# Kernel tuning notes

Measured on AMD Instinct MI355X. Metric: run time of the kernel, lower is better.

## Reference

```python
import jax, jax.numpy as jnp
import numpy as np

NUM_NODES = 100000
NUM_EDGES = 6400000


def setup_inputs() -> dict:
    key = jax.random.key(0)
    k1, k2 = jax.random.split(key)
    e = jax.random.normal(k1, (NUM_EDGES,), dtype=jnp.float32)
    edge_index = jax.random.randint(k2, (2, NUM_EDGES), 0, NUM_NODES, dtype=jnp.int64 if jax.config.jax_enable_x64 else jnp.int32)
    return {"e": e, "edge_index": edge_index, "num_nodes": NUM_NODES}


def reference(e, edge_index, num_nodes):
    # GAT edge softmax (no max-subtraction, matching the 'simple' variant)
    target_nodes = edge_index[1]                      # [E]
    exp_e = jnp.exp(e)                                # [E]
    sum_exp = jax.ops.segment_sum(exp_e, target_nodes, num_segments=num_nodes)  # [N]
    alpha = exp_e / (sum_exp[target_nodes] + 1e-16)   # gather + normalize
    return alpha
```

## Files before the change

kernel.cpp:

```cpp
#include <hip/hip_runtime.h>


typedef unsigned long long ull;

#define NB 25
#define CHUNK_LG 12
#define CHUNK (1 << CHUNK_LG)
#define CCAP (NB * CHUNK)
#define BBLK 512
#define BIN_THREADS 512
#define NSH 2
#define CAP_SH 384
#define BCAP (NSH * CAP_SH)
#define SB 64
#define SRCPG (BBLK / SB)
#define SCB (NB * SB)
#define SCAT_THREADS 256
#define NSUB 8

#define SUMS_OFF 0u
#define FLAG_OFF (448u * 1024u)
#define SUBS_OFF (512u * 1024u)
#define CNTS_OFF (4u << 20)
#define BUF_OFF  (5u << 20)
#define PART_OFF (45u << 20)

__device__ __forceinline__ unsigned short f32_to_f16_bits(float x) {
    union { _Float16 h; unsigned short u; } cv;
    cv.h = (_Float16)x;
    return cv.u;
}
__device__ __forceinline__ float f16_bits_to_f32(unsigned short u) {
    union { unsigned short u; _Float16 h; } cv;
    cv.u = u;
    return (float)cv.h;
}
__device__ __forceinline__ unsigned pack_edge(int t, float x) {
    return ((unsigned)(t & (CHUNK - 1)) << 16) | (unsigned)f32_to_f16_bits(x);
}

__global__ void zero_flag(unsigned* __restrict__ flag) {
    if (threadIdx.x == 0) *flag = 0u;
}

__global__ __launch_bounds__(BIN_THREADS)
void gat_bin(const float* __restrict__ e, const int* __restrict__ tgt,
             unsigned* __restrict__ buf, unsigned* __restrict__ cnts_t,
             unsigned* __restrict__ flag, int per, int E) {
    __shared__ unsigned stage[NB * NSH * CAP_SH];
    __shared__ unsigned lcnt[NB * NSH];
    __shared__ unsigned lovf;
    const int blk = blockIdx.x;
    const int tid = threadIdx.x;
    if (tid < NB * NSH) lcnt[tid] = 0;
    if (tid == 0) lovf = 0;
    __syncthreads();

    const int sh = tid & (NSH - 1);

    const long long start = (long long)blk * per;
    long long rem = (long long)E - start;
    if (rem < 0) rem = 0;
    int nv = per >> 2;
    if ((long long)nv > (rem >> 2)) nv = (int)(rem >> 2);
    const int tail_lo = nv * 4;
    int tail_hi = per;
    if ((long long)tail_hi > rem) tail_hi = (int)rem;

    const float4* e4 = reinterpret_cast<const float4*>(e + start);
    const int4*  t4 = reinterpret_cast<const int4*>(tgt + start);

#define BIN_ONE(T, X)                                                        \
    {   const int t_ = (T);                                                  \
        const unsigned b_ = (unsigned)t_ >> CHUNK_LG;                        \
        if (b_ < NB) {                                                       \
            const unsigned pk_ = pack_edge(t_, __expf(X));                   \
            const unsigned s_ = atomicAdd(&lcnt[b_ * NSH + sh], 1u);         \
            if (s_ < CAP_SH) stage[(b_ * NSH + sh) * CAP_SH + s_] = pk_;     \
            else lovf = 1;                                                   \
        } else lovf = 1;                                                     \
    }
    for (int v = tid; v < nv; v += BIN_THREADS) {
        const float4 ev = e4[v];
        const int4 tv = t4[v];
        BIN_ONE(tv.x, ev.x)
        BIN_ONE(tv.y, ev.y)
        BIN_ONE(tv.z, ev.z)
        BIN_ONE(tv.w, ev.w)
    }
    for (int i = tail_lo + tid; i < tail_hi; i += BIN_THREADS) {
        BIN_ONE(tgt[start + i], e[start + i])
    }
#undef BIN_ONE
    __syncthreads();

#pragma unroll 5
    for (int b = 0; b < NB; ++b) {
        const unsigned c0 = min(lcnt[b * NSH + 0], (unsigned)CAP_SH);
        const unsigned c1 = min(lcnt[b * NSH + 1], (unsigned)CAP_SH);
        unsigned* dst = buf + ((size_t)blk * NB + b) * BCAP;
        const unsigned* s0 = stage + (size_t)(b * NSH + 0) * CAP_SH;
        const unsigned* s1 = stage + (size_t)(b * NSH + 1) * CAP_SH;
        for (unsigned j = tid; j < c0; j += BIN_THREADS) dst[j] = s0[j];
        for (unsigned j = tid; j < c1; j += BIN_THREADS) dst[c0 + j] = s1[j];
        if (tid == 0) cnts_t[b * BBLK + blk] = c0 + c1;
    }
    if (tid == 0 && lovf) atomicOr(flag, 1u);
}

__global__ __launch_bounds__(SCAT_THREADS)
void gat_scatter_bins(const unsigned* __restrict__ buf,
                      const unsigned* __restrict__ cnts_t,
                      unsigned* __restrict__ partials) {
    __shared__ float hist[CHUNK];
    const int blk = blockIdx.x;
    const int b = blk / SB;
    const int g = blk - b * SB;
    const int tid = threadIdx.x;

    const uint4 ca = *(const uint4*)(cnts_t + b * BBLK + g * SRCPG);
    const uint4 cb = *(const uint4*)(cnts_t + b * BBLK + g * SRCPG + 4);
    int ms[SRCPG] = {(int)ca.x, (int)ca.y, (int)ca.z, (int)ca.w,
                     (int)cb.x, (int)cb.y, (int)cb.z, (int)cb.w};

    float4 z; z.x = z.y = z.z = z.w = 0.0f;
#pragma unroll
    for (int j = tid; j < CHUNK / 4; j += SCAT_THREADS)
        ((float4*)hist)[j] = z;
    __syncthreads();

#pragma unroll
    for (int s = 0; s < SRCPG; ++s) {
        const int sb = g * SRCPG + s;
        const int m = ms[s];
        const unsigned* src = buf + ((size_t)sb * NB + b) * BCAP;
        const int nv = m >> 2;
        const uint4* s4 = (const uint4*)src;
        for (int v = tid; v < nv; v += SCAT_THREADS) {
            const uint4 q = s4[v];
            atomicAdd(&hist[q.x >> 16], f16_bits_to_f32((unsigned short)q.x));
            atomicAdd(&hist[q.y >> 16], f16_bits_to_f32((unsigned short)q.y));
            atomicAdd(&hist[q.z >> 16], f16_bits_to_f32((unsigned short)q.z));
            atomicAdd(&hist[q.w >> 16], f16_bits_to_f32((unsigned short)q.w));
        }
        for (int i = nv * 4 + tid; i < m; i += SCAT_THREADS) {
            const unsigned q = src[i];
            atomicAdd(&hist[q >> 16], f16_bits_to_f32((unsigned short)q));
        }
    }
    __syncthreads();

    uint4* dst = (uint4*)(partials + (size_t)blk * (CHUNK / 2));
    const float4* h4 = (const float4*)hist;
#pragma unroll
    for (int j = tid; j < CHUNK / 8; j += SCAT_THREADS) {
        const float4 a = h4[2 * j];
        const float4 c = h4[2 * j + 1];
        uint4 o;
        o.x = (unsigned)f32_to_f16_bits(a.x) | ((unsigned)f32_to_f16_bits(a.y) << 16);
        o.y = (unsigned)f32_to_f16_bits(a.z) | ((unsigned)f32_to_f16_bits(a.w) << 16);
        o.z = (unsigned)f32_to_f16_bits(c.x) | ((unsigned)f32_to_f16_bits(c.y) << 16);
        o.w = (unsigned)f32_to_f16_bits(c.z) | ((unsigned)f32_to_f16_bits(c.w) << 16);
        dst[j] = o;
    }
}

__global__ void gat_reduce1(const unsigned short* __restrict__ partials,
                            float* __restrict__ subsums) {
    const int per_sub = CCAP >> 2;
    const int t = blockIdx.x * blockDim.x + threadIdx.x;
    if (t >= per_sub * NSUB) return;
    const int sub = t / per_sub;
    const int r = t - sub * per_sub;
    const int nd = r << 2;
    const int b = nd >> CHUNK_LG;
    const int w = nd & (CHUNK - 1);
    const int blk0 = b * SB + sub * (SB / NSUB);
    const unsigned short* p = partials + ((size_t)blk0 * CHUNK) + w;
    float a0 = 0.f, a1 = 0.f, a2 = 0.f, a3 = 0.f;
#pragma unroll
    for (int s = 0; s < SB / NSUB; ++s) {
        const ushort4 v = *(const ushort4*)(p + (size_t)s * CHUNK);
        a0 += f16_bits_to_f32(v.x); a1 += f16_bits_to_f32(v.y);
        a2 += f16_bits_to_f32(v.z); a3 += f16_bits_to_f32(v.w);
    }
    float4 o; o.x = a0; o.y = a1; o.z = a2; o.w = a3;
    *(float4*)(subsums + (size_t)sub * CCAP + nd) = o;
}

__global__ void gat_reduce2(const float* __restrict__ subsums,
                            const int* __restrict__ np,
                            float* __restrict__ sums) {
    const int n = *np;
    const int q = blockIdx.x * blockDim.x + threadIdx.x;
    const int nd = q * 4;
    if (nd >= CCAP) return;
    float4 acc; acc.x = acc.y = acc.z = acc.w = 0.f;
#pragma unroll
    for (int s = 0; s < NSUB; ++s) {
        const float4 v = *(const float4*)(subsums + (size_t)s * CCAP + nd);
        acc.x += v.x; acc.y += v.y; acc.z += v.z; acc.w += v.w;
    }
    if (nd + 4 <= n) {
        *(float4*)(sums + nd) = acc;
    } else {
        if (nd     < n) sums[nd]     = acc.x;
        if (nd + 1 < n) sums[nd + 1] = acc.y;
        if (nd + 2 < n) sums[nd + 2] = acc.z;
        if (nd + 3 < n) sums[nd + 3] = acc.w;
    }
}

__global__ void fb_zero(float* __restrict__ sums,
                        const unsigned* __restrict__ flag) {
    if (*flag == 0u) return;
    const int stride = gridDim.x * blockDim.x;
    for (int i = blockIdx.x * blockDim.x + threadIdx.x; i < CCAP; i += stride)
        sums[i] = 0.0f;
}

__global__ void fb_scatter(const float4* __restrict__ e4,
                           const int4* __restrict__ t4,
                           const float* __restrict__ e,
                           const int* __restrict__ tgt,
                           float* __restrict__ sums,
                           const unsigned* __restrict__ flag,
                           int n4, int E) {
    if (*flag == 0u) return;
    const int stride = gridDim.x * blockDim.x;
    const int tid = blockIdx.x * blockDim.x + threadIdx.x;
    for (int i = tid; i < n4; i += stride) {
        const float4 ev = e4[i];
        const int4 tv = t4[i];
        if ((unsigned)tv.x < (unsigned)CCAP) atomicAdd(&sums[tv.x], __expf(ev.x));
        if ((unsigned)tv.y < (unsigned)CCAP) atomicAdd(&sums[tv.y], __expf(ev.y));
        if ((unsigned)tv.z < (unsigned)CCAP) atomicAdd(&sums[tv.z], __expf(ev.z));
        if ((unsigned)tv.w < (unsigned)CCAP) atomicAdd(&sums[tv.w], __expf(ev.w));
    }
    const int tail_base = n4 * 4;
    for (int i = tail_base + tid; i < E; i += stride) {
        const int t = tgt[i];
        if ((unsigned)t < (unsigned)CCAP) atomicAdd(&sums[t], __expf(e[i]));
    }
}

__global__ void gat_zero_sums(float* __restrict__ sums,
                              const int* __restrict__ np) {
    const int n = *np;
    const int stride = gridDim.x * blockDim.x;
    for (int i = blockIdx.x * blockDim.x + threadIdx.x; i < n; i += stride)
        sums[i] = 0.0f;
}

__global__ void gat_exp_scatter(const float4* __restrict__ e4,
                                const int4* __restrict__ t4,
                                const float* __restrict__ e,
                                const int* __restrict__ tgt,
                                float* __restrict__ sums,
                                int n4, int E) {
    const int stride = gridDim.x * blockDim.x;
    const int tid = blockIdx.x * blockDim.x + threadIdx.x;
    for (int i = tid; i < n4; i += stride) {
        const float4 ev = e4[i];
        const int4 tv = t4[i];
        atomicAdd(&sums[tv.x], __expf(ev.x));
        atomicAdd(&sums[tv.y], __expf(ev.y));
        atomicAdd(&sums[tv.z], __expf(ev.z));
        atomicAdd(&sums[tv.w], __expf(ev.w));
    }
    const int tail_base = n4 * 4;
    if (tid < E - tail_base)
        atomicAdd(&sums[tgt[tail_base + tid]], __expf(e[tail_base + tid]));
}

__global__ void gat_normalize(const float4* __restrict__ e4,
                              const int4* __restrict__ t4,
                              const float* __restrict__ e,
                              const int* __restrict__ tgt,
                              const float* __restrict__ sums,
                              float4* __restrict__ out4,
                              float* __restrict__ out,
                              int n4, int E) {
    const int stride = gridDim.x * blockDim.x;
    const int tid = blockIdx.x * blockDim.x + threadIdx.x;
    for (int i = tid; i < n4; i += stride) {
        const float4 ev = e4[i];
        const int4 tv = t4[i];
        float4 r;
        r.x = __expf(ev.x) * __builtin_amdgcn_rcpf(sums[tv.x] + 1e-16f);
        r.y = __expf(ev.y) * __builtin_amdgcn_rcpf(sums[tv.y] + 1e-16f);
        r.z = __expf(ev.z) * __builtin_amdgcn_rcpf(sums[tv.z] + 1e-16f);
        r.w = __expf(ev.w) * __builtin_amdgcn_rcpf(sums[tv.w] + 1e-16f);
        out4[i] = r;
    }
    const int tail_base = n4 * 4;
    if (tid < E - tail_base) {
        const int i = tail_base + tid;
        out[i] = __expf(e[i]) * __builtin_amdgcn_rcpf(sums[tgt[i]] + 1e-16f);
    }
}

extern "C" void kernel_launch(void* const* d_in, const int* in_sizes, int n_in,
                              void* d_out, int out_size, void* d_ws, size_t ws_size,
                              hipStream_t stream) {
    const float* e = (const float*)d_in[0];
    const int* edge_index = (const int*)d_in[1];
    const int* num_nodes_p = (const int*)d_in[2];

    const int E = in_sizes[0];
    const int* tgt = edge_index + E;

    float* sums = (float*)((char*)d_ws + SUMS_OFF);
    float* alpha = (float*)d_out;
    const int n4e = E / 4;

    const int per = (((E + BBLK - 1) / BBLK) + 3) & ~3;

    const size_t need = (size_t)PART_OFF + (size_t)SCB * CHUNK * 2;
    const bool use_bins = ws_size >= need;

    if (use_bins) {
        unsigned* flag = (unsigned*)((char*)d_ws + FLAG_OFF);
        float* subsums = (float*)((char*)d_ws + SUBS_OFF);
        unsigned* cnts_t = (unsigned*)((char*)d_ws + CNTS_OFF);
        unsigned* buf = (unsigned*)((char*)d_ws + BUF_OFF);
        unsigned* part_u32 = (unsigned*)((char*)d_ws + PART_OFF);
        unsigned short* part_u16 = (unsigned short*)part_u32;

        zero_flag<<<1, 64, 0, stream>>>(flag);

        gat_bin<<<BBLK, BIN_THREADS, 0, stream>>>(e, tgt, buf, cnts_t, flag, per, E);

        gat_scatter_bins<<<SCB, SCAT_THREADS, 0, stream>>>(buf, cnts_t, part_u32);

        gat_reduce1<<<(CCAP / 4) * NSUB / 256, 256, 0, stream>>>(part_u16, subsums);

        gat_reduce2<<<(CCAP / 4 + 255) / 256, 256, 0, stream>>>(
            subsums, num_nodes_p, sums);

        fb_zero<<<256, 256, 0, stream>>>(sums, flag);

        fb_scatter<<<1024, 256, 0, stream>>>(
            (const float4*)e, (const int4*)tgt, e, tgt, sums, flag, n4e, E);
    } else {
        gat_zero_sums<<<512, 256, 0, stream>>>(sums, num_nodes_p);
        int blocks = (n4e + 255) / 256;
        if (blocks > 2048) blocks = 2048;
        if (blocks < 1) blocks = 1;
        gat_exp_scatter<<<blocks, 256, 0, stream>>>(
            (const float4*)e, (const int4*)tgt, e, tgt, sums, n4e, E);
    }

    {
        int blocks = (n4e + 255) / 256;
        if (blocks < 1) blocks = 1;
        gat_normalize<<<blocks, 256, 0, stream>>>(
            (const float4*)e, (const int4*)tgt, e, tgt, sums,
            (float4*)alpha, alpha, n4e, E);
    }
}
```

Before: 104.9 us.

## Write binned edges directly to global with fixed-capacity zero-padded slots

The bin kernel stops staging packed edges in LDS and instead writes each edge straight to a fixed-capacity per-(bin,block) slot in global memory. Unused slots are padded with zero-valued entries, so the per-bin count array is no longer needed. The scatter kernel can then stream one contiguous region with a fixed unrolled loop and no count lookup or tail handling. Block count doubles and threads per block halve. This saves LDS traffic and an extra copy pass, but the global writes become scattered and uncoalesced, and the padded entries add wasted shared-memory atomics.

Result: slower. 127.2 us (+21.2%).

```diff
diff --git a/kernel.cpp b/kernel.cpp
--- a/kernel.cpp
+++ b/kernel.cpp
@@ -7,23 +7,21 @@
 #define CHUNK_LG 12
 #define CHUNK (1 << CHUNK_LG)
 #define CCAP (NB * CHUNK)
-#define BBLK 512
-#define BIN_THREADS 512
-#define NSH 2
-#define CAP_SH 384
-#define BCAP (NSH * CAP_SH)
+#define BBLK 1024
+#define BIN_THREADS 256
+#define CAP 352
 #define SB 64
 #define SRCPG (BBLK / SB)
 #define SCB (NB * SB)
 #define SCAT_THREADS 256
+#define STREAM_U4 (SRCPG * CAP / 4)
 #define NSUB 8
 
 #define SUMS_OFF 0u
 #define FLAG_OFF (448u * 1024u)
 #define SUBS_OFF (512u * 1024u)
-#define CNTS_OFF (4u << 20)
-#define BUF_OFF  (5u << 20)
-#define PART_OFF (45u << 20)
+#define BUF_OFF  (4u << 20)
+#define PART_OFF (42u << 20)
 
 __device__ __forceinline__ unsigned short f32_to_f16_bits(float x) {
     union { _Float16 h; unsigned short u; } cv;
@@ -45,18 +43,15 @@
 
 __global__ __launch_bounds__(BIN_THREADS)
 void gat_bin(const float* __restrict__ e, const int* __restrict__ tgt,
-             unsigned* __restrict__ buf, unsigned* __restrict__ cnts_t,
-             unsigned* __restrict__ flag, int per, int E) {
-    __shared__ unsigned stage[NB * NSH * CAP_SH];
-    __shared__ unsigned lcnt[NB * NSH];
+             unsigned* __restrict__ buf, unsigned* __restrict__ flag,
+             int per, int E) {
+    __shared__ unsigned lcnt[NB];
     __shared__ unsigned lovf;
     const int blk = blockIdx.x;
     const int tid = threadIdx.x;
-    if (tid < NB * NSH) lcnt[tid] = 0;
+    if (tid < NB) lcnt[tid] = 0;
     if (tid == 0) lovf = 0;
     __syncthreads();
-
-    const int sh = tid & (NSH - 1);
 
     const long long start = (long long)blk * per;
     long long rem = (long long)E - start;
@@ -75,8 +70,9 @@
         const unsigned b_ = (unsigned)t_ >> CHUNK_LG;                        \
         if (b_ < NB) {                                                       \
             const unsigned pk_ = pack_edge(t_, __expf(X));                   \
-            const unsigned s_ = atomicAdd(&lcnt[b_ * NSH + sh], 1u);         \
-            if (s_ < CAP_SH) stage[(b_ * NSH + sh) * CAP_SH + s_] = pk_;     \
+            const unsigned s_ = atomicAdd(&lcnt[b_], 1u);                    \
+            if (s_ < CAP)                                                    \
+                buf[((size_t)b_ * BBLK + blk) * CAP + s_] = pk_;             \
             else lovf = 1;                                                   \
         } else lovf = 1;                                                     \
     }
@@ -96,21 +92,16 @@
 
 #pragma unroll 5
     for (int b = 0; b < NB; ++b) {
-        const unsigned c0 = min(lcnt[b * NSH + 0], (unsigned)CAP_SH);
-        const unsigned c1 = min(lcnt[b * NSH + 1], (unsigned)CAP_SH);
-        unsigned* dst = buf + ((size_t)blk * NB + b) * BCAP;
-        const unsigned* s0 = stage + (size_t)(b * NSH + 0) * CAP_SH;
-        const unsigned* s1 = stage + (size_t)(b * NSH + 1) * CAP_SH;
-        for (unsigned j = tid; j < c0; j += BIN_THREADS) dst[j] = s0[j];
-        for (unsigned j = tid; j < c1; j += BIN_THREADS) dst[c0 + j] = s1[j];
-        if (tid == 0) cnts_t[b * BBLK + blk] = c0 + c1;
+        const unsigned m = min(lcnt[b], (unsigned)CAP);
+        unsigned* dst = buf + ((size_t)b * BBLK + blk) * CAP;
+        for (unsigned j = m + tid; j < CAP; j += BIN_THREADS)
+            dst[j] = (j & (CHUNK - 1)) << 16;
     }
     if (tid == 0 && lovf) atomicOr(flag, 1u);
 }
 
 __global__ __launch_bounds__(SCAT_THREADS)
 void gat_scatter_bins(const unsigned* __restrict__ buf,
-                      const unsigned* __restrict__ cnts_t,
                       unsigned* __restrict__ partials) {
     __shared__ float hist[CHUNK];
     const int blk = blockIdx.x;
@@ -118,34 +109,23 @@
     const int g = blk - b * SB;
     const int tid = threadIdx.x;
 
-    const uint4 ca = *(const uint4*)(cnts_t + b * BBLK + g * SRCPG);
-    const uint4 cb = *(const uint4*)(cnts_t + b * BBLK + g * SRCPG + 4);
-    int ms[SRCPG] = {(int)ca.x, (int)ca.y, (int)ca.z, (int)ca.w,
-                     (int)cb.x, (int)cb.y, (int)cb.z, (int)cb.w};
-
     float4 z; z.x = z.y = z.z = z.w = 0.0f;
 #pragma unroll
     for (int j = tid; j < CHUNK / 4; j += SCAT_THREADS)
         ((float4*)hist)[j] = z;
     __syncthreads();
 
-#pragma unroll
-    for (int s = 0; s < SRCPG; ++s) {
-        const int sb = g * SRCPG + s;
-        const int m = ms[s];
-        const unsigned* src = buf + ((size_t)sb * NB + b) * BCAP;
-        const int nv = m >> 2;
-        const uint4* s4 = (const uint4*)src;
-        for (int v = tid; v < nv; v += SCAT_THREADS) {
+    const uint4* s4 = reinterpret_cast<const uint4*>(
+        buf + ((size_t)b * BBLK + (size_t)g * SRCPG) * CAP);
+#pragma unroll
+    for (int k = 0; k < 6; ++k) {
+        const int v = tid + k * SCAT_THREADS;
+        if (v < STREAM_U4) {
             const uint4 q = s4[v];
             atomicAdd(&hist[q.x >> 16], f16_bits_to_f32((unsigned short)q.x));
             atomicAdd(&hist[q.y >> 16], f16_bits_to_f32((unsigned short)q.y));
             atomicAdd(&hist[q.z >> 16], f16_bits_to_f32((unsigned short)q.z));
             atomicAdd(&hist[q.w >> 16], f16_bits_to_f32((unsigned short)q.w));
-        }
-        for (int i = nv * 4 + tid; i < m; i += SCAT_THREADS) {
-            const unsigned q = src[i];
-            atomicAdd(&hist[q >> 16], f16_bits_to_f32((unsigned short)q));
         }
     }
     __syncthreads();
@@ -322,16 +302,15 @@
     if (use_bins) {
         unsigned* flag = (unsigned*)((char*)d_ws + FLAG_OFF);
         float* subsums = (float*)((char*)d_ws + SUBS_OFF);
-        unsigned* cnts_t = (unsigned*)((char*)d_ws + CNTS_OFF);
         unsigned* buf = (unsigned*)((char*)d_ws + BUF_OFF);
         unsigned* part_u32 = (unsigned*)((char*)d_ws + PART_OFF);
         unsigned short* part_u16 = (unsigned short*)part_u32;
 
         zero_flag<<<1, 64, 0, stream>>>(flag);
 
-        gat_bin<<<BBLK, BIN_THREADS, 0, stream>>>(e, tgt, buf, cnts_t, flag, per, E);
-
-        gat_scatter_bins<<<SCB, SCAT_THREADS, 0, stream>>>(buf, cnts_t, part_u32);
+        gat_bin<<<BBLK, BIN_THREADS, 0, stream>>>(e, tgt, buf, flag, per, E);
+
+        gat_scatter_bins<<<SCB, SCAT_THREADS, 0, stream>>>(buf, part_u32);
 
         gat_reduce1<<<(CCAP / 4) * NSUB / 256, 256, 0, stream>>>(part_u16, subsums);
 
```
